# Optimization experiments

Hardware: AMD Instinct MI355X
Metric: run time of the kernel (lower is better)

## Reference

```python
import jax, jax.numpy as jnp
import numpy as np

B, S, HID, NH = 2, 2048, 2048, 16
ROPE, NOPE, VDIM = 64, 64, 128
QHEAD = ROPE + NOPE            # 128
QLORA = HID // 3               # 682
KVLORA = HID // 8              # 256
THETA = 128000.0
SCALE = 1.0 / np.sqrt(QHEAD)   # deepseek softmax_scale = q_head_dim**-0.5
EPS = 1e-6


def rmsnorm(x, w):
    var = jnp.mean(x.astype(jnp.float32) ** 2, axis=-1, keepdims=True)
    return (x.astype(jnp.float32) * jax.lax.rsqrt(var + EPS)).astype(x.dtype) * w


def rope_cos_sin(seq, dim, theta):
    inv = 1.0 / (theta ** (jnp.arange(0, dim, 2, dtype=jnp.float32) / dim))
    t = jnp.arange(seq, dtype=jnp.float32)
    freqs = jnp.outer(t, inv)                      # [S, dim/2]
    emb = jnp.concatenate([freqs, freqs], axis=-1)  # [S, dim]
    return jnp.cos(emb), jnp.sin(emb)


def apply_rope(x, cos, sin):
    # deepseek interleave: view(b,h,s,d/2,2).transpose(-1,-2).reshape, then rotate_half rope
    b, h, s, d = x.shape
    x = x.reshape(b, h, s, d // 2, 2).transpose(0, 1, 2, 4, 3).reshape(b, h, s, d)
    x1, x2 = jnp.split(x, 2, axis=-1)
    rot = jnp.concatenate([-x2, x1], axis=-1)
    return x * cos + rot * sin


def setup_inputs() -> dict:
    key = jax.random.key(0)
    ks = jax.random.split(key, 8)
    s = lambda fan_in: 1.0 / np.sqrt(fan_in)
    return {
        "x":        jax.random.normal(ks[0], (B, S, HID), jnp.float32),
        "q_a_w":    jax.random.normal(ks[1], (HID, QLORA), jnp.float32) * s(HID),
        "q_a_ln_w": jnp.ones((QLORA,), jnp.float32),
        "q_b_w":    jax.random.normal(ks[2], (QLORA, NH * QHEAD), jnp.float32) * s(QLORA),
        "kv_a_w":   jax.random.normal(ks[3], (HID, KVLORA + ROPE), jnp.float32) * s(HID),
        "kv_a_ln_w": jnp.ones((KVLORA,), jnp.float32),
        "kv_b_w":   jax.random.normal(ks[4], (KVLORA, NH * (NOPE + VDIM)), jnp.float32) * s(KVLORA),
        "o_w":      jax.random.normal(ks[5], (NH * VDIM, HID), jnp.float32) * s(NH * VDIM),
    }


def reference(x, q_a_w, q_a_ln_w, q_b_w, kv_a_w, kv_a_ln_w, kv_b_w, o_w):
    b, s, _ = x.shape
    # Q: low-rank down-proj -> RMSNorm -> up-proj
    q = rmsnorm(x @ q_a_w, q_a_ln_w) @ q_b_w               # [b,s,NH*QHEAD]
    q = q.reshape(b, s, NH, QHEAD).transpose(0, 2, 1, 3)   # [b,NH,s,QHEAD]
    q_nope, q_pe = q[..., :NOPE], q[..., NOPE:]
    # KV: compressed latent + shared rope key
    ckv_kpe = x @ kv_a_w                                   # [b,s,KVLORA+ROPE]
    ckv, k_pe = ckv_kpe[..., :KVLORA], ckv_kpe[..., KVLORA:]
    k_pe = k_pe.reshape(b, 1, s, ROPE)                     # shared across heads
    kv = rmsnorm(ckv, kv_a_ln_w) @ kv_b_w                  # [b,s,NH*(NOPE+VDIM)]
    kv = kv.reshape(b, s, NH, NOPE + VDIM).transpose(0, 2, 1, 3)
    k_nope, v = kv[..., :NOPE], kv[..., NOPE:]             # [b,NH,s,NOPE], [b,NH,s,VDIM]
    # decoupled RoPE on the rope split only
    cos, sin = rope_cos_sin(s, ROPE, THETA)
    q_pe = apply_rope(q_pe, cos, sin)
    k_pe = apply_rope(k_pe, cos, sin)
    qf = jnp.concatenate([q_nope, q_pe], axis=-1)          # [b,NH,s,QHEAD]
    kf = jnp.concatenate([k_nope, jnp.broadcast_to(k_pe, (b, NH, s, ROPE))], axis=-1)
    scores = jnp.einsum('bhqd,bhkd->bhqk', qf, kf) * SCALE
    causal = jnp.tril(jnp.ones((s, s), bool))
    scores = jnp.where(causal, scores, jnp.float32(-1e9))
    attn = jax.nn.softmax(scores.astype(jnp.float32), axis=-1).astype(qf.dtype)
    out = jnp.einsum('bhqk,bhkd->bhqd', attn, v)           # [b,NH,s,VDIM]
    out = out.transpose(0, 2, 1, 3).reshape(b, s, NH * VDIM)
    return out @ o_w                                       # [b,s,HID]
```

## Files before the change

kernel.cpp:

```cpp
#include <hip/hip_runtime.h>
#include <hip/hip_bf16.h>

typedef __attribute__((ext_vector_type(8))) short short8;
typedef __attribute__((ext_vector_type(4))) float f32x4;

using bf16 = __hip_bfloat16;

static constexpr int B_ = 2, S_ = 2048, HID_ = 2048, NH_ = 16;
static constexpr int ROPE_ = 64, VDIM_ = 128, QHEAD_ = 128;
static constexpr int QLORA_ = 682, KVLORA_ = 256;
static constexpr int QLORA_P = 704;
static constexpr int NQA_P = 768;
static constexpr int NKVA_P = 384;
static constexpr int NA_ = NQA_P + NKVA_P;
static constexpr float THETA_ = 128000.0f;
static constexpr float SCALE_ = 0.08838834764831845f;
static constexpr float SCL2_ = 0.08838834764831845f * 1.4426950408889634f;
static constexpr float EPS_ = 1e-6f;
static constexpr int BS_ = B_ * S_;

__device__ __forceinline__ void gl2lds16(const void* g, void* l) {
    __builtin_amdgcn_global_load_lds(
        (const __attribute__((address_space(1))) unsigned int*)g,
        (__attribute__((address_space(3))) unsigned int*)l, 16, 0, 0);
}

struct bf16x4_s { bf16 x, y, z, w; };

__device__ __forceinline__ float bfLo(unsigned int u) { return __uint_as_float(u << 16); }
__device__ __forceinline__ float bfHi(unsigned int u) { return __uint_as_float(u & 0xffff0000u); }

struct TD { const float* src; bf16* dst; const float* colw;
            int Ksrc, Nsrc, Kpad, tilesX, off, perm; };
struct TDs { TD d[5]; };
static constexpr int PREP_TILES = 8576;

__global__ void k_prep(TDs P, const float* __restrict__ x, bf16* __restrict__ xb,
                       float* __restrict__ ct, float* __restrict__ st) {
    __shared__ float tile[32][33];
    if (blockIdx.x >= PREP_TILES) {
        int bid = blockIdx.x - PREP_TILES;
        int t = threadIdx.y * 32 + threadIdx.x;
        if (bid < 8192) {
            int i = bid * 256 + t;
            float4 v = reinterpret_cast<const float4*>(x)[i];
            bf16x4_s o;
            o.x = __float2bfloat16(v.x); o.y = __float2bfloat16(v.y);
            o.z = __float2bfloat16(v.z); o.w = __float2bfloat16(v.w);
            reinterpret_cast<bf16x4_s*>(xb)[i] = o;
        } else {
            int idx = (bid - 8192) * 256 + t;
            int tpos = idx >> 5, j = idx & 31;
            float inv = expf(-(float)j * (logf(THETA_) / 32.0f));
            float f = (float)tpos * inv;
            ct[idx] = cosf(f);
            st[idx] = sinf(f);
        }
        return;
    }
    int flat = blockIdx.x;
    int di = 0;
    #pragma unroll
    for (int i = 1; i < 5; ++i) if (flat >= P.d[i].off) di = i;
    TD d = P.d[di];
    int local = flat - d.off;
    int xt = local % d.tilesX, yt = local / d.tilesX;
    int kb = xt * 32, nb = yt * 32;
    int tx = threadIdx.x, ty = threadIdx.y;
    #pragma unroll
    for (int i = 0; i < 32; i += 8) {
        int k = kb + ty + i, n = nb + tx;
        float v = (k < d.Ksrc && n < d.Nsrc) ? d.src[(size_t)k * d.Nsrc + n] : 0.0f;
        if (d.colw && k < d.Ksrc) v *= d.colw[k];
        tile[ty + i][tx] = v;
    }
    __syncthreads();
    int u = ty * 32 + tx;
    int kp = u & 15;
    int nl = u >> 4;
    #pragma unroll
    for (int half = 0; half < 2; ++half) {
        int n_loc = nl + 16 * half;
        int n = nb + n_loc;
        int nd = n;
        if (d.perm) {
            int h = n / 192, dd = n - h * 192;
            nd = (dd < 64) ? h * 64 + dd : 1024 + h * 128 + (dd - 64);
        }
        bf16 lo = __float2bfloat16(tile[2 * kp][n_loc]);
        bf16 hi = __float2bfloat16(tile[2 * kp + 1][n_loc]);
        unsigned int pk = (unsigned int)*reinterpret_cast<unsigned short*>(&lo) |
                          ((unsigned int)*reinterpret_cast<unsigned short*>(&hi) << 16);
        *reinterpret_cast<unsigned int*>(d.dst + (size_t)nd * d.Kpad + kb + 2 * kp) = pk;
    }
}

#define GEMM_VARS                                                                        \
    __shared__ bf16 As[128 * 64];                                                        \
    __shared__ bf16 Bs[128 * 64];                                                        \
    const int t = threadIdx.x;                                                           \
    const int lane = t & 63, w = t >> 6;                                                 \
    const int l15 = lane & 15, l4 = lane >> 4;                                           \
    const int wr = (w >> 1) * 64, wc = (w & 1) * 64;

#define GEMM_CORE(Aptr, Bptr, LDA, LDB, KDIM, M0V, N0V)                                  \
    const int m0 = (M0V), n0 = (N0V);                                                    \
    f32x4 acc[4][4] = {};                                                                \
    for (int k0 = 0; k0 < (KDIM); k0 += 64) {                                            \
        _Pragma("unroll")                                                                \
        for (int i = 0; i < 4; ++i) {                                                    \
            int cid = t + i * 256;                                                       \
            int row = cid >> 3;                                                          \
            int ch = (cid & 7) ^ (row & 7);                                              \
            gl2lds16((Aptr) + (size_t)(m0 + row) * (LDA) + k0 + ch * 8,                  \
                     reinterpret_cast<char*>(As) + cid * 16);                            \
            gl2lds16((Bptr) + (size_t)(n0 + row) * (LDB) + k0 + ch * 8,                  \
                     reinterpret_cast<char*>(Bs) + cid * 16);                            \
        }                                                                                \
        __syncthreads();                                                                 \
        _Pragma("unroll")                                                                \
        for (int kk = 0; kk < 2; ++kk) {                                                 \
            short8 a[4], b[4];                                                           \
            _Pragma("unroll")                                                            \
            for (int m = 0; m < 4; ++m) {                                                \
                int row = wr + m * 16 + l15;                                             \
                int ch = (kk * 4 + l4) ^ (row & 7);                                      \
                a[m] = *reinterpret_cast<const short8*>(                                 \
                    reinterpret_cast<const char*>(As) + row * 128 + ch * 16);            \
            }                                                                            \
            _Pragma("unroll")                                                            \
            for (int n = 0; n < 4; ++n) {                                                \
                int row = wc + n * 16 + l15;                                             \
                int ch = (kk * 4 + l4) ^ (row & 7);                                      \
                b[n] = *reinterpret_cast<const short8*>(                                 \
                    reinterpret_cast<const char*>(Bs) + row * 128 + ch * 16);            \
            }                                                                            \
            _Pragma("unroll")                                                            \
            for (int m = 0; m < 4; ++m)                                                  \
                _Pragma("unroll")                                                        \
                for (int n = 0; n < 4; ++n)                                              \
                    acc[m][n] = __builtin_amdgcn_mfma_f32_16x16x32_bf16(a[m], b[n],      \
                                                                       acc[m][n], 0, 0, 0); \
        }                                                                                \
        __syncthreads();                                                                 \
    }

template <typename OutT>
__launch_bounds__(256)
__global__ void gemm_bt(const bf16* __restrict__ A, const bf16* __restrict__ Bt,
                        OutT* __restrict__ C, int K, int lda, int ldb, int ldc)
{
    GEMM_VARS
    GEMM_CORE(A, Bt, lda, ldb, K, blockIdx.y * 128, blockIdx.x * 128)
    #pragma unroll
    for (int m = 0; m < 4; ++m)
        #pragma unroll
        for (int n = 0; n < 4; ++n)
            #pragma unroll
            for (int j = 0; j < 4; ++j) {
                int r = m0 + wr + m * 16 + l4 * 4 + j;
                int c = n0 + wc + n * 16 + l15;
                float v = acc[m][n][j];
                if constexpr (sizeof(OutT) == 2) C[(size_t)r * ldc + c] = __float2bfloat16(v);
                else                             C[(size_t)r * ldc + c] = v;
            }
}

__launch_bounds__(256)
__global__ void gemm_a(const bf16* __restrict__ A, const bf16* __restrict__ Bt,
                       bf16* __restrict__ qac,
                       const float* __restrict__ ct, const float* __restrict__ st,
                       bf16* __restrict__ kr)
{
    GEMM_VARS
    GEMM_CORE(A, Bt, HID_, HID_, HID_, blockIdx.y * 128, blockIdx.x * 128)
    if (n0 < 1024) {
        #pragma unroll
        for (int m = 0; m < 4; ++m)
            #pragma unroll
            for (int n = 0; n < 4; ++n)
                #pragma unroll
                for (int j = 0; j < 4; ++j) {
                    int r = m0 + wr + m * 16 + l4 * 4 + j;
                    int c = n0 + wc + n * 16 + l15;
                    qac[(size_t)r * NA_ + c] = __float2bfloat16(acc[m][n][j]);
                }
    } else if (wc == 0) {
        #pragma unroll
        for (int m = 0; m < 4; ++m)
            #pragma unroll
            for (int n = 0; n < 4; ++n)
                #pragma unroll
                for (int j = 0; j < 4; ++j) {
                    int r = m0 + wr + m * 16 + l4 * 4 + j;
                    int p = n * 16 + l15;
                    int jj = p >> 1, odd = p & 1;
                    float v = acc[m][n][j];
                    float pr = __shfl_xor(v, 1);
                    float e0 = odd ? pr : v, e1 = odd ? v : pr;
                    int s = r & (S_ - 1);
                    float c_ = ct[s * 32 + jj], s_ = st[s * 32 + jj];
                    float ov = odd ? (e1 * c_ + e0 * s_) : (e0 * c_ - e1 * s_);
                    kr[(size_t)r * 64 + (odd ? 32 : 0) + jj] = __float2bfloat16(ov);
                }
    }
}

__launch_bounds__(256)
__global__ void k_scales(const bf16* __restrict__ qac,
                         float* __restrict__ qs, float* __restrict__ ks)
{
    __shared__ float red[8];
    int bs = blockIdx.x;
    int t = threadIdx.x, lane = t & 63, w = t >> 6;
    const unsigned int* qp = reinterpret_cast<const unsigned int*>(qac + (size_t)bs * NA_);
    float sq = 0.f, sk = 0.f;
    for (int p = t; p < 341; p += 256) {
        unsigned int u = qp[p];
        float a = bfLo(u), b = bfHi(u);
        sq += a * a + b * b;
    }
    if (t < 128) {
        unsigned int u = qp[384 + t];
        float a = bfLo(u), b = bfHi(u);
        sk = a * a + b * b;
    }
    #pragma unroll
    for (int m = 1; m < 64; m <<= 1) { sq += __shfl_xor(sq, m); sk += __shfl_xor(sk, m); }
    if (lane == 0) { red[w] = sq; red[4 + w] = sk; }
    __syncthreads();
    if (t == 0) {
        sq = red[0] + red[1] + red[2] + red[3];
        sk = red[4] + red[5] + red[6] + red[7];
        qs[bs] = rsqrtf(sq / (float)QLORA_ + EPS_);
        ks[bs] = rsqrtf(sk / (float)KVLORA_ + EPS_);
    }
}

__launch_bounds__(256)
__global__ void gemm_up(const bf16* __restrict__ qac, const bf16* __restrict__ qb_wt,
                        const float* __restrict__ ct, const float* __restrict__ st,
                        const float* __restrict__ qs, bf16* __restrict__ Qf,
                        const bf16* __restrict__ kvb_wt, const float* __restrict__ ks,
                        bf16* __restrict__ knope, bf16* __restrict__ Vt)
{
    GEMM_VARS
    if (blockIdx.x < 16) {
        GEMM_CORE(qac, qb_wt, NA_, QLORA_P, QLORA_P, blockIdx.y * 128, blockIdx.x * 128)
        (void)n0;
        const int h = blockIdx.x;
        if (wc == 0) {
            #pragma unroll
            for (int m = 0; m < 4; ++m) {
                int rb = m0 + wr + m * 16 + l4 * 4;
                float q4[4];
                #pragma unroll
                for (int j = 0; j < 4; ++j) q4[j] = qs[rb + j] * SCL2_;
                #pragma unroll
                for (int n = 0; n < 4; ++n)
                    #pragma unroll
                    for (int j = 0; j < 4; ++j) {
                        int r = rb + j;
                        int c = n * 16 + l15;
                        int s = r & (S_ - 1), bq = r >> 11;
                        Qf[((size_t)(bq * NH_ + h) * S_ + s) * 128 + c] =
                            __float2bfloat16(acc[m][n][j] * q4[j]);
                    }
            }
        } else {
            #pragma unroll
            for (int m = 0; m < 4; ++m) {
                int rb = m0 + wr + m * 16 + l4 * 4;
                float q4[4];
                #pragma unroll
                for (int j = 0; j < 4; ++j) q4[j] = qs[rb + j] * SCL2_;
                #pragma unroll
                for (int n = 0; n < 4; ++n)
                    #pragma unroll
                    for (int j = 0; j < 4; ++j) {
                        int r = rb + j;
                        int p = n * 16 + l15;
                        int jj = p >> 1, odd = p & 1;
                        float v = acc[m][n][j];
                        float pr = __shfl_xor(v, 1);
                        float e0 = odd ? pr : v, e1 = odd ? v : pr;
                        int s = r & (S_ - 1), bq = r >> 11;
                        float c_ = ct[s * 32 + jj], s_ = st[s * 32 + jj];
                        float ov = odd ? (e1 * c_ + e0 * s_) : (e0 * c_ - e1 * s_);
                        int c_out = 64 + (odd ? 32 : 0) + jj;
                        Qf[((size_t)(bq * NH_ + h) * S_ + s) * 128 + c_out] =
                            __float2bfloat16(ov * q4[j]);
                    }
            }
        }
    } else {
        GEMM_CORE(qac + NQA_P, kvb_wt, NA_, KVLORA_, KVLORA_, blockIdx.y * 128,
                  (blockIdx.x - 16) * 128)
        if (n0 < 1024) {
            #pragma unroll
            for (int m = 0; m < 4; ++m) {
                int rb = m0 + wr + m * 16 + l4 * 4;
                float k4[4];
                #pragma unroll
                for (int j = 0; j < 4; ++j) k4[j] = ks[rb + j];
                #pragma unroll
                for (int n = 0; n < 4; ++n)
                    #pragma unroll
                    for (int j = 0; j < 4; ++j) {
                        int c = n0 + wc + n * 16 + l15;
                        knope[(size_t)(rb + j) * 1024 + c] =
                            __float2bfloat16(acc[m][n][j] * k4[j]);
                    }
            }
        } else {
            const int h = (n0 - 1024) >> 7;
            const int bq = m0 >> 11;
            const int bh = bq * NH_ + h;
            #pragma unroll
            for (int m = 0; m < 4; ++m) {
                int rb = m0 + wr + m * 16 + l4 * 4;
                int s = rb & (S_ - 1);
                float k4[4];
                #pragma unroll
                for (int j = 0; j < 4; ++j) k4[j] = ks[rb + j];
                #pragma unroll
                for (int n = 0; n < 4; ++n) {
                    int cl = wc + n * 16 + l15;
                    ushort4 pk;
                    {
                        bf16 h0 = __float2bfloat16(acc[m][n][0] * k4[0]);
                        bf16 h1 = __float2bfloat16(acc[m][n][1] * k4[1]);
                        bf16 h2 = __float2bfloat16(acc[m][n][2] * k4[2]);
                        bf16 h3 = __float2bfloat16(acc[m][n][3] * k4[3]);
                        pk.x = *reinterpret_cast<unsigned short*>(&h0);
                        pk.y = *reinterpret_cast<unsigned short*>(&h1);
                        pk.z = *reinterpret_cast<unsigned short*>(&h2);
                        pk.w = *reinterpret_cast<unsigned short*>(&h3);
                    }
                    *reinterpret_cast<ushort4*>(Vt + ((size_t)bh * 128 + cl) * S_ + s) = pk;
                }
            }
        }
    }
}

__launch_bounds__(256, 4)
__global__ void k_flash(const bf16* __restrict__ Qf, const bf16* __restrict__ knope,
                        const bf16* __restrict__ kr, const bf16* __restrict__ Vt,
                        bf16* __restrict__ attn_out)
{
    __shared__ bf16 Ks[64 * 128];
    __shared__ bf16 Vs[128 * 64];
    __shared__ bf16 Ps[4][16 * 64];

    const int t = threadIdx.x, lane = t & 63, w = t >> 6;
    const int l15 = lane & 15, l4 = lane >> 4;
    const int strip = 31 - blockIdx.y;
    const int bh = blockIdx.x;
    const int b = bh >> 4, h = bh & 15;
    const int r0 = strip * 64 + w * 16;
    const int NT = strip + 1;

    short8 qa_[4];
    {
        const bf16* qrow = Qf + ((size_t)bh * S_ + r0 + l15) * 128;
        #pragma unroll
        for (int kk = 0; kk < 4; ++kk)
            qa_[kk] = *reinterpret_cast<const short8*>(qrow + kk * 32 + l4 * 8);
    }

    const bf16* kS[4]; size_t kStep[4];
    const bf16* vS[4];
    #pragma unroll
    for (int i = 0; i < 4; ++i) {
        int cid = t + i * 256;
        int row = cid >> 4, ch = (cid & 15) ^ (row & 7);
        kS[i] = (ch < 8) ? knope + (size_t)(b * S_ + row) * 1024 + h * 64 + ch * 8
                         : kr + (size_t)(b * S_ + row) * 64 + (ch - 8) * 8;
        kStep[i] = (ch < 8) ? (size_t)64 * 1024 : (size_t)64 * 64;
    }
    {
        const bf16* Vg = Vt + (size_t)bh * 128 * S_;
        #pragma unroll
        for (int i = 0; i < 4; ++i) {
            int cid = t + i * 256;
            int row = cid >> 3, ch = (cid & 7) ^ (row & 7);
            vS[i] = Vg + (size_t)row * S_ + ch * 8;
        }
    }
    auto stage = [&]() {
        #pragma unroll
        for (int i = 0; i < 4; ++i) {
            gl2lds16(kS[i], reinterpret_cast<char*>(Ks) + (t + i * 256) * 16);
            kS[i] += kStep[i];
        }
        #pragma unroll
        for (int i = 0; i < 4; ++i) {
            gl2lds16(vS[i], reinterpret_cast<char*>(Vs) + (t + i * 256) * 16);
            vS[i] += 64;
        }
    };

    stage();

    f32x4 o[8] = {};
    float m_r = -1e30f, l_r = 0.f;

    for (int kb = 0; kb < NT; ++kb) {
        const int k0 = kb * 64;
        __syncthreads();

        f32x4 sfr[4] = {};
        __builtin_amdgcn_s_setprio(1);
        #pragma unroll
        for (int kk = 0; kk < 4; ++kk) {
            short8 kf[4];
            #pragma unroll
            for (int m = 0; m < 4; ++m) {
                int row = m * 16 + l15;
                int ch = (kk * 4 + l4) ^ (row & 7);
                kf[m] = *reinterpret_cast<const short8*>(
                    reinterpret_cast<const char*>(Ks) + row * 256 + ch * 16);
            }
            #pragma unroll
            for (int m = 0; m < 4; ++m)
                sfr[m] = __builtin_amdgcn_mfma_f32_16x16x32_bf16(kf[m], qa_[kk], sfr[m], 0, 0, 0);
        }
        __builtin_amdgcn_s_setprio(0);

        const int qrow = r0 + l15;
        if (k0 + 63 > r0) {
            #pragma unroll
            for (int m = 0; m < 4; ++m) {
                int kbase = k0 + m * 16 + l4 * 4;
                #pragma unroll
                for (int j = 0; j < 4; ++j)
                    if (kbase + j > qrow) sfr[m][j] = -1e30f;
            }
        }

        float rm;
        {
            float a0 = fmaxf(fmaxf(sfr[0][0], sfr[0][1]), fmaxf(sfr[0][2], sfr[0][3]));
            float a1 = fmaxf(fmaxf(sfr[1][0], sfr[1][1]), fmaxf(sfr[1][2], sfr[1][3]));
            float a2 = fmaxf(fmaxf(sfr[2][0], sfr[2][1]), fmaxf(sfr[2][2], sfr[2][3]));
            float a3 = fmaxf(fmaxf(sfr[3][0], sfr[3][1]), fmaxf(sfr[3][2], sfr[3][3]));
            rm = fmaxf(fmaxf(a0, a1), fmaxf(a2, a3));
        }
        rm = fmaxf(rm, __shfl_xor(rm, 16));
        rm = fmaxf(rm, __shfl_xor(rm, 32));

        if (__ballot(rm > m_r + 8.0f)) {
            float mn = fmaxf(m_r, rm);
            float alpha = exp2f(m_r - mn);
            m_r = mn;
            l_r *= alpha;
            float aj[4];
            #pragma unroll
            for (int j = 0; j < 4; ++j) aj[j] = __shfl(alpha, l4 * 4 + j);
            #pragma unroll
            for (int n = 0; n < 8; ++n)
                #pragma unroll
                for (int j = 0; j < 4; ++j) o[n][j] *= aj[j];
        }

        char* pb = reinterpret_cast<char*>(Ps[w]);
        float rs = 0.f;
        #pragma unroll
        for (int m = 0; m < 4; ++m) {
            float p0 = exp2f(sfr[m][0] - m_r);
            float p1 = exp2f(sfr[m][1] - m_r);
            float p2 = exp2f(sfr[m][2] - m_r);
            float p3 = exp2f(sfr[m][3] - m_r);
            rs += (p0 + p1) + (p2 + p3);
            union { __hip_bfloat162 h; unsigned int u; } cl, ch2;
            cl.h  = __float22bfloat162_rn(make_float2(p0, p1));
            ch2.h = __float22bfloat162_rn(make_float2(p2, p3));
            int kloc = m * 16 + l4 * 4;
            int chnk = (kloc >> 3) ^ (l15 & 7);
            uint2 pk2; pk2.x = cl.u; pk2.y = ch2.u;
            *reinterpret_cast<uint2*>(pb + l15 * 128 + chnk * 16 + (kloc & 7) * 2) = pk2;
        }
        rs += __shfl_xor(rs, 16);
        rs += __shfl_xor(rs, 32);
        l_r += rs;

        __builtin_amdgcn_s_setprio(1);
        #pragma unroll
        for (int kk = 0; kk < 2; ++kk) {
            int pch = (kk * 4 + l4) ^ (l15 & 7);
            short8 pa = *reinterpret_cast<const short8*>(pb + l15 * 128 + pch * 16);
            #pragma unroll
            for (int n = 0; n < 8; ++n) {
                int row = n * 16 + l15;
                int ch = (kk * 4 + l4) ^ (row & 7);
                short8 vb = *reinterpret_cast<const short8*>(
                    reinterpret_cast<const char*>(Vs) + row * 128 + ch * 16);
                o[n] = __builtin_amdgcn_mfma_f32_16x16x32_bf16(pa, vb, o[n], 0, 0, 0);
            }
        }
        __builtin_amdgcn_s_setprio(0);

        __syncthreads();
        if (kb + 1 < NT) stage();
    }

    float rj[4];
    #pragma unroll
    for (int j = 0; j < 4; ++j) rj[j] = __builtin_amdgcn_rcpf(__shfl(l_r, l4 * 4 + j));
    size_t obase = ((size_t)(b * S_) + r0) * (size_t)(NH_ * VDIM_) + h * VDIM_;
    #pragma unroll
    for (int n = 0; n < 8; ++n)
        #pragma unroll
        for (int j = 0; j < 4; ++j) {
            int r = l4 * 4 + j;
            int c = n * 16 + l15;
            attn_out[obase + (size_t)r * (NH_ * VDIM_) + c] = __float2bfloat16(o[n][j] * rj[j]);
        }
}

extern "C" void kernel_launch(void* const* d_in, const int* in_sizes, int n_in,
                              void* d_out, int out_size, void* d_ws, size_t ws_size,
                              hipStream_t stream)
{
    (void)in_sizes; (void)n_in; (void)out_size;
    const float* x       = (const float*)d_in[0];
    const float* q_a_w   = (const float*)d_in[1];
    const float* q_a_ln  = (const float*)d_in[2];
    const float* q_b_w   = (const float*)d_in[3];
    const float* kv_a_w  = (const float*)d_in[4];
    const float* kv_a_ln = (const float*)d_in[5];
    const float* kv_b_w  = (const float*)d_in[6];
    const float* o_w     = (const float*)d_in[7];
    float* out = (float*)d_out;

    char* ws = (char*)d_ws;
    size_t off = 0;
    auto alloc = [&](size_t bytes) -> char* {
        char* p = ws + off;
        off += (bytes + 255) & ~(size_t)255;
        return p;
    };

    bf16* xb     = (bf16*)alloc((size_t)BS_ * HID_ * 2);
    bf16* a_wt   = (bf16*)alloc((size_t)NA_ * HID_ * 2);
    bf16* qb_wt  = (bf16*)alloc((size_t)2048 * QLORA_P * 2);
    bf16* kvb_wt = (bf16*)alloc((size_t)3072 * KVLORA_ * 2);
    bf16* ow_t   = (bf16*)alloc((size_t)2048 * 2048 * 2);
    float* ct    = (float*)alloc((size_t)S_ * 32 * 4);
    float* st    = (float*)alloc((size_t)S_ * 32 * 4);
    bf16* qac    = (bf16*)alloc((size_t)BS_ * NA_ * 2);
    float* qs    = (float*)alloc((size_t)BS_ * 4);
    float* ksc   = (float*)alloc((size_t)BS_ * 4);
    bf16* kr     = (bf16*)alloc((size_t)BS_ * 64 * 2);
    bf16* knope  = (bf16*)alloc((size_t)BS_ * 1024 * 2);
    bf16* Vt     = (bf16*)alloc((size_t)BS_ * 2048 * 2);
    bf16* attn   = (bf16*)alloc((size_t)BS_ * 2048 * 2);

    bf16* Qf = xb;

    if (ws_size < off) return;

    TDs P;
    P.d[0] = TD{ q_a_w,  a_wt,                     nullptr, 2048,  682, 2048, 64,    0, 0 };
    P.d[1] = TD{ kv_a_w, a_wt + (size_t)NQA_P*2048,nullptr, 2048,  320, 2048, 64, 1536, 0 };
    P.d[2] = TD{ q_b_w,  qb_wt,                    q_a_ln,   682, 2048,  704, 22, 2304, 0 };
    P.d[3] = TD{ kv_b_w, kvb_wt,                   kv_a_ln,  256, 3072,  256,  8, 3712, 1 };
    P.d[4] = TD{ o_w,    ow_t,                     nullptr, 2048, 2048, 2048, 64, 4480, 0 };
    k_prep<<<PREP_TILES + 8192 + 256, dim3(32, 8), 0, stream>>>(P, x, xb, ct, st);

    gemm_a<<<dim3(NA_ / 128, BS_ / 128), 256, 0, stream>>>(xb, a_wt, qac, ct, st, kr);

    k_scales<<<BS_, 256, 0, stream>>>(qac, qs, ksc);

    gemm_up<<<dim3(16 + 24, BS_ / 128), 256, 0, stream>>>(qac, qb_wt, ct, st, qs, Qf,
                                                          kvb_wt, ksc, knope, Vt);

    k_flash<<<dim3(B_ * NH_, 32), 256, 0, stream>>>(Qf, knope, kr, Vt, attn);

    gemm_bt<float><<<dim3(2048 / 128, BS_ / 128), 256, 0, stream>>>(attn, ow_t, out,
                                                                    HID_, HID_, HID_, 2048);
}
```

Baseline: 223.1 us.

## Load K and V fragments directly from global memory in flash attention

After: 518.9 us. +132.5%, slower.

```diff
diff --git a/kernel.cpp b/kernel.cpp
--- a/kernel.cpp
+++ b/kernel.cpp
@@ -349,8 +349,6 @@
                         const bf16* __restrict__ kr, const bf16* __restrict__ Vt,
                         bf16* __restrict__ attn_out)
 {
-    __shared__ bf16 Ks[64 * 128];
-    __shared__ bf16 Vs[128 * 64];
     __shared__ bf16 Ps[4][16 * 64];
 
     const int t = threadIdx.x, lane = t & 63, w = t >> 6;
@@ -369,64 +367,51 @@
             qa_[kk] = *reinterpret_cast<const short8*>(qrow + kk * 32 + l4 * 8);
     }
 
-    const bf16* kS[4]; size_t kStep[4];
-    const bf16* vS[4];
-    #pragma unroll
-    for (int i = 0; i < 4; ++i) {
-        int cid = t + i * 256;
-        int row = cid >> 4, ch = (cid & 15) ^ (row & 7);
-        kS[i] = (ch < 8) ? knope + (size_t)(b * S_ + row) * 1024 + h * 64 + ch * 8
-                         : kr + (size_t)(b * S_ + row) * 64 + (ch - 8) * 8;
-        kStep[i] = (ch < 8) ? (size_t)64 * 1024 : (size_t)64 * 64;
-    }
-    {
-        const bf16* Vg = Vt + (size_t)bh * 128 * S_;
-        #pragma unroll
-        for (int i = 0; i < 4; ++i) {
-            int cid = t + i * 256;
-            int row = cid >> 3, ch = (cid & 7) ^ (row & 7);
-            vS[i] = Vg + (size_t)row * S_ + ch * 8;
-        }
-    }
-    auto stage = [&]() {
-        #pragma unroll
-        for (int i = 0; i < 4; ++i) {
-            gl2lds16(kS[i], reinterpret_cast<char*>(Ks) + (t + i * 256) * 16);
-            kS[i] += kStep[i];
-        }
-        #pragma unroll
-        for (int i = 0; i < 4; ++i) {
-            gl2lds16(vS[i], reinterpret_cast<char*>(Vs) + (t + i * 256) * 16);
-            vS[i] += 64;
-        }
-    };
-
-    stage();
+    const bf16* Kn = knope + (size_t)(b * S_) * 1024 + h * 64;
+    const bf16* Kr = kr + (size_t)(b * S_) * 64;
+    const bf16* Vg = Vt + (size_t)bh * 128 * S_;
+    int oKn[4], oKr[4], oV[8];
+    #pragma unroll
+    for (int m = 0; m < 4; ++m) {
+        oKn[m] = (m * 16 + l15) * 1024 + l4 * 8;
+        oKr[m] = (m * 16 + l15) * 64 + l4 * 8;
+    }
+    #pragma unroll
+    for (int n = 0; n < 8; ++n) oV[n] = (n * 16 + l15) * S_ + l4 * 8;
 
     f32x4 o[8] = {};
     float m_r = -1e30f, l_r = 0.f;
 
     for (int kb = 0; kb < NT; ++kb) {
         const int k0 = kb * 64;
-        __syncthreads();
 
         f32x4 sfr[4] = {};
-        __builtin_amdgcn_s_setprio(1);
-        #pragma unroll
-        for (int kk = 0; kk < 4; ++kk) {
-            short8 kf[4];
+        {
+            short8 kf0[4], kf1[4], kf2[4], kf3[4];
             #pragma unroll
             for (int m = 0; m < 4; ++m) {
-                int row = m * 16 + l15;
-                int ch = (kk * 4 + l4) ^ (row & 7);
-                kf[m] = *reinterpret_cast<const short8*>(
-                    reinterpret_cast<const char*>(Ks) + row * 256 + ch * 16);
-            }
+                kf0[m] = *reinterpret_cast<const short8*>(Kn + oKn[m]);
+                kf1[m] = *reinterpret_cast<const short8*>(Kn + oKn[m] + 32);
+                kf2[m] = *reinterpret_cast<const short8*>(Kr + oKr[m]);
+                kf3[m] = *reinterpret_cast<const short8*>(Kr + oKr[m] + 32);
+            }
+            __builtin_amdgcn_s_setprio(1);
             #pragma unroll
             for (int m = 0; m < 4; ++m)
-                sfr[m] = __builtin_amdgcn_mfma_f32_16x16x32_bf16(kf[m], qa_[kk], sfr[m], 0, 0, 0);
-        }
-        __builtin_amdgcn_s_setprio(0);
+                sfr[m] = __builtin_amdgcn_mfma_f32_16x16x32_bf16(kf0[m], qa_[0], sfr[m], 0, 0, 0);
+            #pragma unroll
+            for (int m = 0; m < 4; ++m)
+                sfr[m] = __builtin_amdgcn_mfma_f32_16x16x32_bf16(kf1[m], qa_[1], sfr[m], 0, 0, 0);
+            #pragma unroll
+            for (int m = 0; m < 4; ++m)
+                sfr[m] = __builtin_amdgcn_mfma_f32_16x16x32_bf16(kf2[m], qa_[2], sfr[m], 0, 0, 0);
+            #pragma unroll
+            for (int m = 0; m < 4; ++m)
+                sfr[m] = __builtin_amdgcn_mfma_f32_16x16x32_bf16(kf3[m], qa_[3], sfr[m], 0, 0, 0);
+            __builtin_amdgcn_s_setprio(0);
+        }
+        #pragma unroll
+        for (int m = 0; m < 4; ++m) { oKn[m] += 64 * 1024; oKr[m] += 64 * 64; }
 
         const int qrow = r0 + l15;
         if (k0 + 63 > r0) {
@@ -492,17 +477,15 @@
             short8 pa = *reinterpret_cast<const short8*>(pb + l15 * 128 + pch * 16);
             #pragma unroll
             for (int n = 0; n < 8; ++n) {
-                int row = n * 16 + l15;
-                int ch = (kk * 4 + l4) ^ (row & 7);
-                short8 vb = *reinterpret_cast<const short8*>(
-                    reinterpret_cast<const char*>(Vs) + row * 128 + ch * 16);
+                short8 vb = (kk == 0)
+                    ? *reinterpret_cast<const short8*>(Vg + oV[n])
+                    : *reinterpret_cast<const short8*>(Vg + oV[n] + 32);
                 o[n] = __builtin_amdgcn_mfma_f32_16x16x32_bf16(pa, vb, o[n], 0, 0, 0);
             }
         }
         __builtin_amdgcn_s_setprio(0);
-
-        __syncthreads();
-        if (kb + 1 < NT) stage();
+        #pragma unroll
+        for (int n = 0; n < 8; ++n) oV[n] += 64;
     }
 
     float rj[4];
```

## Pair causal query strips in one flash block to share K/V tiles

Applied to the files above, without the earlier changes.

After: 218.3 us. -2.2%, faster.

```diff
diff --git a/kernel.cpp b/kernel.cpp
--- a/kernel.cpp
+++ b/kernel.cpp
@@ -344,22 +344,23 @@
     }
 }
 
-__launch_bounds__(256, 4)
+__launch_bounds__(512, 4)
 __global__ void k_flash(const bf16* __restrict__ Qf, const bf16* __restrict__ knope,
                         const bf16* __restrict__ kr, const bf16* __restrict__ Vt,
                         bf16* __restrict__ attn_out)
 {
     __shared__ bf16 Ks[64 * 128];
     __shared__ bf16 Vs[128 * 64];
-    __shared__ bf16 Ps[4][16 * 64];
+    __shared__ bf16 Ps[8][16 * 64];
 
     const int t = threadIdx.x, lane = t & 63, w = t >> 6;
     const int l15 = lane & 15, l4 = lane >> 4;
-    const int strip = 31 - blockIdx.y;
+    const int pi = blockIdx.y;
     const int bh = blockIdx.x;
     const int b = bh >> 4, h = bh & 15;
-    const int r0 = strip * 64 + w * 16;
-    const int NT = strip + 1;
+    const int strip = (w < 4) ? (31 - pi) : pi;
+    const int r0 = strip * 64 + (w & 3) * 16;
+    const int NT = 32 - pi;
 
     short8 qa_[4];
     {
@@ -369,36 +370,33 @@
             qa_[kk] = *reinterpret_cast<const short8*>(qrow + kk * 32 + l4 * 8);
     }
 
-    const bf16* kS[4]; size_t kStep[4];
-    const bf16* vS[4];
-    #pragma unroll
-    for (int i = 0; i < 4; ++i) {
-        int cid = t + i * 256;
-        int row = cid >> 4, ch = (cid & 15) ^ (row & 7);
-        kS[i] = (ch < 8) ? knope + (size_t)(b * S_ + row) * 1024 + h * 64 + ch * 8
+    const bf16 *kSrc0, *kSrc1, *vSrc0, *vSrc1;
+    size_t kStp0, kStp1;
+    {
+        int cid = t, row = cid >> 4, ch = (cid & 15) ^ (row & 7);
+        kSrc0 = (ch < 8) ? knope + (size_t)(b * S_ + row) * 1024 + h * 64 + ch * 8
                          : kr + (size_t)(b * S_ + row) * 64 + (ch - 8) * 8;
-        kStep[i] = (ch < 8) ? (size_t)64 * 1024 : (size_t)64 * 64;
+        kStp0 = (ch < 8) ? (size_t)64 * 1024 : (size_t)64 * 64;
+    }
+    {
+        int cid = t + 512, row = cid >> 4, ch = (cid & 15) ^ (row & 7);
+        kSrc1 = (ch < 8) ? knope + (size_t)(b * S_ + row) * 1024 + h * 64 + ch * 8
+                         : kr + (size_t)(b * S_ + row) * 64 + (ch - 8) * 8;
+        kStp1 = (ch < 8) ? (size_t)64 * 1024 : (size_t)64 * 64;
     }
     {
         const bf16* Vg = Vt + (size_t)bh * 128 * S_;
-        #pragma unroll
-        for (int i = 0; i < 4; ++i) {
-            int cid = t + i * 256;
-            int row = cid >> 3, ch = (cid & 7) ^ (row & 7);
-            vS[i] = Vg + (size_t)row * S_ + ch * 8;
-        }
+        int cid = t, row = cid >> 3, ch = (cid & 7) ^ (row & 7);
+        vSrc0 = Vg + (size_t)row * S_ + ch * 8;
+        cid = t + 512; row = cid >> 3; ch = (cid & 7) ^ (row & 7);
+        vSrc1 = Vg + (size_t)row * S_ + ch * 8;
     }
     auto stage = [&]() {
-        #pragma unroll
-        for (int i = 0; i < 4; ++i) {
-            gl2lds16(kS[i], reinterpret_cast<char*>(Ks) + (t + i * 256) * 16);
-            kS[i] += kStep[i];
-        }
-        #pragma unroll
-        for (int i = 0; i < 4; ++i) {
-            gl2lds16(vS[i], reinterpret_cast<char*>(Vs) + (t + i * 256) * 16);
-            vS[i] += 64;
-        }
+        gl2lds16(kSrc0, reinterpret_cast<char*>(Ks) + t * 16);
+        gl2lds16(kSrc1, reinterpret_cast<char*>(Ks) + (t + 512) * 16);
+        gl2lds16(vSrc0, reinterpret_cast<char*>(Vs) + t * 16);
+        gl2lds16(vSrc1, reinterpret_cast<char*>(Vs) + (t + 512) * 16);
+        kSrc0 += kStp0; kSrc1 += kStp1; vSrc0 += 64; vSrc1 += 64;
     };
 
     stage();
@@ -410,97 +408,98 @@
         const int k0 = kb * 64;
         __syncthreads();
 
-        f32x4 sfr[4] = {};
-        __builtin_amdgcn_s_setprio(1);
-        #pragma unroll
-        for (int kk = 0; kk < 4; ++kk) {
-            short8 kf[4];
+        if (k0 <= r0 + 15) {
+            f32x4 sfr[4] = {};
+            __builtin_amdgcn_s_setprio(1);
+            #pragma unroll
+            for (int kk = 0; kk < 4; ++kk) {
+                short8 kf[4];
+                #pragma unroll
+                for (int m = 0; m < 4; ++m) {
+                    int row = m * 16 + l15;
+                    int ch = (kk * 4 + l4) ^ (row & 7);
+                    kf[m] = *reinterpret_cast<const short8*>(
+                        reinterpret_cast<const char*>(Ks) + row * 256 + ch * 16);
+                }
+                #pragma unroll
+                for (int m = 0; m < 4; ++m)
+                    sfr[m] = __builtin_amdgcn_mfma_f32_16x16x32_bf16(kf[m], qa_[kk], sfr[m], 0, 0, 0);
+            }
+            __builtin_amdgcn_s_setprio(0);
+
+            const int qrow = r0 + l15;
+            if (k0 + 63 > r0) {
+                #pragma unroll
+                for (int m = 0; m < 4; ++m) {
+                    int kbase = k0 + m * 16 + l4 * 4;
+                    #pragma unroll
+                    for (int j = 0; j < 4; ++j)
+                        if (kbase + j > qrow) sfr[m][j] = -1e30f;
+                }
+            }
+
+            float rm;
+            {
+                float a0 = fmaxf(fmaxf(sfr[0][0], sfr[0][1]), fmaxf(sfr[0][2], sfr[0][3]));
+                float a1 = fmaxf(fmaxf(sfr[1][0], sfr[1][1]), fmaxf(sfr[1][2], sfr[1][3]));
+                float a2 = fmaxf(fmaxf(sfr[2][0], sfr[2][1]), fmaxf(sfr[2][2], sfr[2][3]));
+                float a3 = fmaxf(fmaxf(sfr[3][0], sfr[3][1]), fmaxf(sfr[3][2], sfr[3][3]));
+                rm = fmaxf(fmaxf(a0, a1), fmaxf(a2, a3));
+            }
+            rm = fmaxf(rm, __shfl_xor(rm, 16));
+            rm = fmaxf(rm, __shfl_xor(rm, 32));
+
+            if (__ballot(rm > m_r + 8.0f)) {
+                float mn = fmaxf(m_r, rm);
+                float alpha = exp2f(m_r - mn);
+                m_r = mn;
+                l_r *= alpha;
+                float aj[4];
+                #pragma unroll
+                for (int j = 0; j < 4; ++j) aj[j] = __shfl(alpha, l4 * 4 + j);
+                #pragma unroll
+                for (int n = 0; n < 8; ++n)
+                    #pragma unroll
+                    for (int j = 0; j < 4; ++j) o[n][j] *= aj[j];
+            }
+
+            char* pb = reinterpret_cast<char*>(Ps[w]);
+            float rs = 0.f;
             #pragma unroll
             for (int m = 0; m < 4; ++m) {
-                int row = m * 16 + l15;
-                int ch = (kk * 4 + l4) ^ (row & 7);
-                kf[m] = *reinterpret_cast<const short8*>(
-                    reinterpret_cast<const char*>(Ks) + row * 256 + ch * 16);
-            }
-            #pragma unroll
-            for (int m = 0; m < 4; ++m)
-                sfr[m] = __builtin_amdgcn_mfma_f32_16x16x32_bf16(kf[m], qa_[kk], sfr[m], 0, 0, 0);
+                float p0 = exp2f(sfr[m][0] - m_r);
+                float p1 = exp2f(sfr[m][1] - m_r);
+                float p2 = exp2f(sfr[m][2] - m_r);
+                float p3 = exp2f(sfr[m][3] - m_r);
+                rs += (p0 + p1) + (p2 + p3);
+                union { __hip_bfloat162 h; unsigned int u; } cl, ch2;
+                cl.h  = __float22bfloat162_rn(make_float2(p0, p1));
+                ch2.h = __float22bfloat162_rn(make_float2(p2, p3));
+                int kloc = m * 16 + l4 * 4;
+                int chnk = (kloc >> 3) ^ (l15 & 7);
+                uint2 pk2; pk2.x = cl.u; pk2.y = ch2.u;
+                *reinterpret_cast<uint2*>(pb + l15 * 128 + chnk * 16 + (kloc & 7) * 2) = pk2;
+            }
+            rs += __shfl_xor(rs, 16);
+            rs += __shfl_xor(rs, 32);
+            l_r += rs;
+
+            __builtin_amdgcn_s_setprio(1);
+            #pragma unroll
+            for (int kk = 0; kk < 2; ++kk) {
+                int pch = (kk * 4 + l4) ^ (l15 & 7);
+                short8 pa = *reinterpret_cast<const short8*>(pb + l15 * 128 + pch * 16);
+                #pragma unroll
+                for (int n = 0; n < 8; ++n) {
+                    int row = n * 16 + l15;
+                    int ch = (kk * 4 + l4) ^ (row & 7);
+                    short8 vb = *reinterpret_cast<const short8*>(
+                        reinterpret_cast<const char*>(Vs) + row * 128 + ch * 16);
+                    o[n] = __builtin_amdgcn_mfma_f32_16x16x32_bf16(pa, vb, o[n], 0, 0, 0);
+                }
+            }
+            __builtin_amdgcn_s_setprio(0);
         }
-        __builtin_amdgcn_s_setprio(0);
-
-        const int qrow = r0 + l15;
-        if (k0 + 63 > r0) {
-            #pragma unroll
-            for (int m = 0; m < 4; ++m) {
-                int kbase = k0 + m * 16 + l4 * 4;
-                #pragma unroll
-                for (int j = 0; j < 4; ++j)
-                    if (kbase + j > qrow) sfr[m][j] = -1e30f;
-            }
-        }
-
-        float rm;
-        {
-            float a0 = fmaxf(fmaxf(sfr[0][0], sfr[0][1]), fmaxf(sfr[0][2], sfr[0][3]));
-            float a1 = fmaxf(fmaxf(sfr[1][0], sfr[1][1]), fmaxf(sfr[1][2], sfr[1][3]));
-            float a2 = fmaxf(fmaxf(sfr[2][0], sfr[2][1]), fmaxf(sfr[2][2], sfr[2][3]));
-            float a3 = fmaxf(fmaxf(sfr[3][0], sfr[3][1]), fmaxf(sfr[3][2], sfr[3][3]));
-            rm = fmaxf(fmaxf(a0, a1), fmaxf(a2, a3));
-        }
-        rm = fmaxf(rm, __shfl_xor(rm, 16));
-        rm = fmaxf(rm, __shfl_xor(rm, 32));
-
-        if (__ballot(rm > m_r + 8.0f)) {
-            float mn = fmaxf(m_r, rm);
-            float alpha = exp2f(m_r - mn);
-            m_r = mn;
-            l_r *= alpha;
-            float aj[4];
-            #pragma unroll
-            for (int j = 0; j < 4; ++j) aj[j] = __shfl(alpha, l4 * 4 + j);
-            #pragma unroll
-            for (int n = 0; n < 8; ++n)
-                #pragma unroll
-                for (int j = 0; j < 4; ++j) o[n][j] *= aj[j];
-        }
-
-        char* pb = reinterpret_cast<char*>(Ps[w]);
-        float rs = 0.f;
-        #pragma unroll
-        for (int m = 0; m < 4; ++m) {
-            float p0 = exp2f(sfr[m][0] - m_r);
-            float p1 = exp2f(sfr[m][1] - m_r);
-            float p2 = exp2f(sfr[m][2] - m_r);
-            float p3 = exp2f(sfr[m][3] - m_r);
-            rs += (p0 + p1) + (p2 + p3);
-            union { __hip_bfloat162 h; unsigned int u; } cl, ch2;
-            cl.h  = __float22bfloat162_rn(make_float2(p0, p1));
-            ch2.h = __float22bfloat162_rn(make_float2(p2, p3));
-            int kloc = m * 16 + l4 * 4;
-            int chnk = (kloc >> 3) ^ (l15 & 7);
-            uint2 pk2; pk2.x = cl.u; pk2.y = ch2.u;
-            *reinterpret_cast<uint2*>(pb + l15 * 128 + chnk * 16 + (kloc & 7) * 2) = pk2;
-        }
-        rs += __shfl_xor(rs, 16);
-        rs += __shfl_xor(rs, 32);
-        l_r += rs;
-
-        __builtin_amdgcn_s_setprio(1);
-        #pragma unroll
-        for (int kk = 0; kk < 2; ++kk) {
-            int pch = (kk * 4 + l4) ^ (l15 & 7);
-            short8 pa = *reinterpret_cast<const short8*>(pb + l15 * 128 + pch * 16);
-            #pragma unroll
-            for (int n = 0; n < 8; ++n) {
-                int row = n * 16 + l15;
-                int ch = (kk * 4 + l4) ^ (row & 7);
-                short8 vb = *reinterpret_cast<const short8*>(
-                    reinterpret_cast<const char*>(Vs) + row * 128 + ch * 16);
-                o[n] = __builtin_amdgcn_mfma_f32_16x16x32_bf16(pa, vb, o[n], 0, 0, 0);
-            }
-        }
-        __builtin_amdgcn_s_setprio(0);
-
         __syncthreads();
         if (kb + 1 < NT) stage();
     }
@@ -576,7 +575,7 @@
     gemm_up<<<dim3(16 + 24, BS_ / 128), 256, 0, stream>>>(qac, qb_wt, ct, st, qs, Qf,
                                                           kvb_wt, ksc, knope, Vt);
 
-    k_flash<<<dim3(B_ * NH_, 32), 256, 0, stream>>>(Qf, knope, kr, Vt, attn);
+    k_flash<<<dim3(B_ * NH_, 16), 512, 0, stream>>>(Qf, knope, kr, Vt, attn);
 
     gemm_bt<float><<<dim3(2048 / 128, BS_ / 128), 256, 0, stream>>>(attn, ow_t, out,
                                                                     HID_, HID_, HID_, 2048);
```
